# Kernel optimization log

Hardware: AMD Instinct MI355X
Metric: run time of the kernel (lower is better)

## Reference

```python
import jax, jax.numpy as jnp
import numpy as np

KERNEL = 8
WEIGHT_INIT = np.array([0.49403, -0.44625, 0.82544, 0.99267, 1.6915, -2.0835, 2.9114,
                        -5.6555, 3.5984, -10.205, 20.828, -0.0022237, 0.0097854, 157.35],
                       dtype=np.float32)


def setup_inputs() -> dict:
    key = jax.random.key(0)
    x = jax.random.normal(key, (2048, 128, KERNEL, KERNEL), dtype=jnp.float32)
    weight = jnp.asarray(WEIGHT_INIT)
    return {"input": x, "weight": weight}


def reference(input, weight):
    eye = jnp.eye(KERNEL, dtype=input.dtype)  # serves as both mask and eye(8)
    # A = I - x @ x^T  over trailing two dims
    A = eye - jnp.matmul(input, jnp.swapaxes(input, 2, 3))
    B = jnp.matmul(A, A)
    C = jnp.matmul(B, A)
    D = jnp.matmul(C, A)
    E = jnp.matmul(D, A)
    F = jnp.matmul(E, A)
    G = jnp.matmul(F, A)
    Mat = (weight[0] * A + weight[1] * B + weight[2] * C + weight[3] * D
           + weight[4] * E + weight[5] * F + weight[6] * G + weight[7] * eye)
    return input + jnp.matmul(Mat, input)
```

## Files before the change

### kernel.cpp

```cpp
#include <hip/hip_runtime.h>


typedef float v2f __attribute__((ext_vector_type(2)));

__device__ __forceinline__ v2f pk_mul(v2f a, v2f b) {
    v2f d;
    asm("v_pk_mul_f32 %0, %1, %2" : "=v"(d) : "v"(a), "v"(b));
    return d;
}
__device__ __forceinline__ void pk_fma(v2f &acc, v2f a, v2f b) {
    asm("v_pk_fma_f32 %0, %1, %2, %0" : "+v"(acc) : "v"(a), "v"(b));
}
__device__ __forceinline__ v2f pk_mul_lo(v2f a, v2f b) {
    v2f d;
    asm("v_pk_mul_f32 %0, %1, %2 op_sel:[0,0] op_sel_hi:[0,1]"
        : "=v"(d) : "v"(a), "v"(b));
    return d;
}
__device__ __forceinline__ void pk_fma_lo(v2f &acc, v2f a, v2f b) {
    asm("v_pk_fma_f32 %0, %1, %2, %0 op_sel:[0,0,0] op_sel_hi:[0,1,1]"
        : "+v"(acc) : "v"(a), "v"(b));
}
__device__ __forceinline__ void pk_fma_hi(v2f &acc, v2f a, v2f b) {
    asm("v_pk_fma_f32 %0, %1, %2, %0 op_sel:[1,0,0] op_sel_hi:[1,1,1]"
        : "+v"(acc) : "v"(a), "v"(b));
}

__device__ __forceinline__ float pswap(float x)
{
    return __builtin_bit_cast(float,
        __builtin_amdgcn_update_dpp(0, __builtin_bit_cast(int, x),
                                    0xB1, 0xF, 0xF, true));
}

#define SE(p, q) S[(p) < (q) ? (p) : (q)][(p) < (q) ? (q) : (p)]
#define AE(p, q) A[(p) < (q) ? (p) : (q)][(p) < (q) ? (q) : (p)]

#define POW_STEP(wk)                                                      \
    {                                                                     \
        const v2f wv = (v2f){(wk), (wk)};                                 \
        _Pragma("unroll")                                                 \
        for (int j = 0; j < 2; ++j) {                                     \
            v2f n[8];                                                     \
            _Pragma("unroll")                                             \
            for (int p = 0; p < 8; ++p) {                                 \
                v2f a = pk_mul_lo(Ar[p][0], y[j][0]);                     \
                pk_fma_hi(a, Ar[p][0], y[j][1]);                          \
                pk_fma_lo(a, Ar[p][1], y[j][2]);                          \
                pk_fma_hi(a, Ar[p][1], y[j][3]);                          \
                pk_fma_lo(a, Ar[p][2], y[j][4]);                          \
                pk_fma_hi(a, Ar[p][2], y[j][5]);                          \
                pk_fma_lo(a, Ar[p][3], y[j][6]);                          \
                pk_fma_hi(a, Ar[p][3], y[j][7]);                          \
                n[p] = a;                                                 \
            }                                                             \
            _Pragma("unroll")                                             \
            for (int p = 0; p < 8; ++p) {                                 \
                y[j][p] = n[p];                                           \
                pk_fma(acc[j][p], wv, n[p]);                              \
            }                                                             \
        }                                                                 \
    }

__global__ __launch_bounds__(256)
__attribute__((amdgpu_waves_per_eu(2, 8)))
void ns_poly_kernel(const float* __restrict__ in,
                    const float* __restrict__ wp,
                    float* __restrict__ out)
{
    const int tid = threadIdx.x;
    const int m   = blockIdx.x * 128 + (tid >> 1);
    const int h   = tid & 1;

    const float w0 = wp[0], w1 = wp[1], w2 = wp[2], w3 = wp[3];
    const float w4 = wp[4], w5 = wp[5], w6 = wp[6], w7 = wp[7];

    const float* bp      = in + (size_t)m * 64 + h * 4;
    const float* baseOwn = bp + h * 32;
    const float* basePar = bp + (1 - h) * 32;

    v2f y[2][8];
#pragma unroll
    for (int p = 0; p < 4; ++p) {
        const float4 v = *reinterpret_cast<const float4*>(baseOwn + p * 8);
        y[0][p] = (v2f){v.x, v.y};
        y[1][p] = (v2f){v.z, v.w};
    }
#pragma unroll
    for (int p = 0; p < 4; ++p) {
        const float4 v = *reinterpret_cast<const float4*>(basePar + p * 8);
        y[0][4 + p] = (v2f){v.x, v.y};
        y[1][4 + p] = (v2f){v.z, v.w};
    }

    float S[8][8];
#pragma unroll
    for (int p = 0; p < 8; ++p)
#pragma unroll
        for (int q = p; q < 8; ++q) {
            v2f a = pk_mul(y[0][p], y[0][q]);
            pk_fma(a, y[1][p], y[1][q]);
            S[p][q] = a.x + a.y;
        }

    float A[8][8];
#pragma unroll
    for (int p = 0; p < 8; ++p)
#pragma unroll
        for (int q = p; q < 8; ++q) {
            const float other = pswap(SE((p) ^ 4, (q) ^ 4));
            A[p][q] = (p == q ? 1.0f : 0.0f) - S[p][q] - other;
        }

    v2f Ar[8][4];
#pragma unroll
    for (int p = 0; p < 8; ++p)
#pragma unroll
        for (int jq = 0; jq < 4; ++jq)
            Ar[p][jq] = (v2f){AE(p, 2 * jq), AE(p, 2 * jq + 1)};

    v2f acc[2][8];
    const v2f w7v = (v2f){1.0f + w7, 1.0f + w7};
#pragma unroll
    for (int j = 0; j < 2; ++j)
#pragma unroll
        for (int p = 0; p < 8; ++p)
            acc[j][p] = pk_mul(w7v, y[j][p]);

    POW_STEP(w0);
    POW_STEP(w1);
    POW_STEP(w2);
    POW_STEP(w3);
    POW_STEP(w4);
    POW_STEP(w5);
    POW_STEP(w6);

    float* obp     = out + (size_t)m * 64 + h * 4;
    float* oandOwn = obp + h * 32;
    float* oandPar = obp + (1 - h) * 32;
#pragma unroll
    for (int p = 0; p < 4; ++p)
        *reinterpret_cast<float4*>(oandOwn + p * 8) =
            make_float4(acc[0][p].x, acc[0][p].y, acc[1][p].x, acc[1][p].y);
#pragma unroll
    for (int p = 0; p < 4; ++p)
        *reinterpret_cast<float4*>(oandPar + p * 8) =
            make_float4(acc[0][4 + p].x, acc[0][4 + p].y,
                        acc[1][4 + p].x, acc[1][4 + p].y);
}

extern "C" void kernel_launch(void* const* d_in, const int* in_sizes, int n_in,
                              void* d_out, int out_size, void* d_ws, size_t ws_size,
                              hipStream_t stream)
{
    const float* in = (const float*)d_in[0];
    const float* w  = (const float*)d_in[1];
    float* outp     = (float*)d_out;

    const int nmat   = in_sizes[0] / 64;
    const int blocks = nmat / 128;
    ns_poly_kernel<<<blocks, 256, 0, stream>>>(in, w, outp);
}
```

Before: 126.6 us.

## Stage input and output through swizzled LDS for coalesced global access

Each wave now copies its 32 matrices into LDS with fully contiguous float4 global loads, then reads its per-lane row pairs from LDS using an XOR swizzle. The output is staged the same way in reverse. Rows are now read in natural order instead of own/partner order, which simplifies the partner index in the A construction. The goal is to replace strided per-thread global loads and stores with coalesced ones, at the cost of 32KB of LDS per block. The waves_per_eu attribute is also removed, and the LDS handoff depends on lgkmcnt waits within a wave instead of barriers.

After: 119.6 us. -5.5%, faster.

```diff
diff --git a/kernel.cpp b/kernel.cpp
--- a/kernel.cpp
+++ b/kernel.cpp
@@ -33,7 +33,6 @@
                                     0xB1, 0xF, 0xF, true));
 }
 
-#define SE(p, q) S[(p) < (q) ? (p) : (q)][(p) < (q) ? (q) : (p)]
 #define AE(p, q) A[(p) < (q) ? (p) : (q)][(p) < (q) ? (q) : (p)]
 
 #define POW_STEP(wk)                                                      \
@@ -63,34 +62,43 @@
     }
 
 __global__ __launch_bounds__(256)
-__attribute__((amdgpu_waves_per_eu(2, 8)))
 void ns_poly_kernel(const float* __restrict__ in,
                     const float* __restrict__ wp,
                     float* __restrict__ out)
 {
-    const int tid = threadIdx.x;
-    const int m   = blockIdx.x * 128 + (tid >> 1);
-    const int h   = tid & 1;
+    __shared__ float4 lds[2048];
+
+    const int tid  = threadIdx.x;
+    const int wave = tid >> 6;
+    const int lane = tid & 63;
+    const int l    = lane >> 1;
+    const int h    = lane & 1;
 
     const float w0 = wp[0], w1 = wp[1], w2 = wp[2], w3 = wp[3];
     const float w4 = wp[4], w5 = wp[5], w6 = wp[6], w7 = wp[7];
 
-    const float* bp      = in + (size_t)m * 64 + h * 4;
-    const float* baseOwn = bp + h * 32;
-    const float* basePar = bp + (1 - h) * 32;
+    const int wave_mat0 = blockIdx.x * 128 + wave * 32;
+    const float4* __restrict__ gsrc =
+        reinterpret_cast<const float4*>(in) + (size_t)wave_mat0 * 16;
+    float4* __restrict__ gdst =
+        reinterpret_cast<float4*>(out) + (size_t)wave_mat0 * 16;
+    float4* L = lds + wave * 512;
+
+#pragma unroll
+    for (int it = 0; it < 8; ++it) {
+        const int C  = it * 64 + lane;
+        const int Cs = C ^ (((C >> 4) & 3) << 1);
+        L[Cs] = gsrc[C];
+    }
+    asm volatile("s_waitcnt lgkmcnt(0)" ::: "memory");
 
     v2f y[2][8];
 #pragma unroll
-    for (int p = 0; p < 4; ++p) {
-        const float4 v = *reinterpret_cast<const float4*>(baseOwn + p * 8);
-        y[0][p] = (v2f){v.x, v.y};
-        y[1][p] = (v2f){v.z, v.w};
-    }
-#pragma unroll
-    for (int p = 0; p < 4; ++p) {
-        const float4 v = *reinterpret_cast<const float4*>(basePar + p * 8);
-        y[0][4 + p] = (v2f){v.x, v.y};
-        y[1][4 + p] = (v2f){v.z, v.w};
+    for (int g = 0; g < 8; ++g) {
+        const int f4 = (l * 16 + g * 2 + h) ^ ((l & 3) << 1);
+        const float4 v = L[f4];
+        y[0][g] = (v2f){v.x, v.y};
+        y[1][g] = (v2f){v.z, v.w};
     }
 
     float S[8][8];
@@ -108,7 +116,7 @@
     for (int p = 0; p < 8; ++p)
 #pragma unroll
         for (int q = p; q < 8; ++q) {
-            const float other = pswap(SE((p) ^ 4, (q) ^ 4));
+            const float other = pswap(S[p][q]);
             A[p][q] = (p == q ? 1.0f : 0.0f) - S[p][q] - other;
         }
 
@@ -135,18 +143,20 @@
     POW_STEP(w5);
     POW_STEP(w6);
 
-    float* obp     = out + (size_t)m * 64 + h * 4;
-    float* oandOwn = obp + h * 32;
-    float* oandPar = obp + (1 - h) * 32;
 #pragma unroll
-    for (int p = 0; p < 4; ++p)
-        *reinterpret_cast<float4*>(oandOwn + p * 8) =
-            make_float4(acc[0][p].x, acc[0][p].y, acc[1][p].x, acc[1][p].y);
+    for (int g = 0; g < 8; ++g) {
+        const int f4 = (l * 16 + g * 2 + h) ^ ((l & 3) << 1);
+        L[f4] = make_float4(acc[0][g].x, acc[0][g].y,
+                            acc[1][g].x, acc[1][g].y);
+    }
+    asm volatile("s_waitcnt lgkmcnt(0)" ::: "memory");
+
 #pragma unroll
-    for (int p = 0; p < 4; ++p)
-        *reinterpret_cast<float4*>(oandPar + p * 8) =
-            make_float4(acc[0][4 + p].x, acc[0][4 + p].y,
-                        acc[1][4 + p].x, acc[1][4 + p].y);
+    for (int it = 0; it < 8; ++it) {
+        const int C  = it * 64 + lane;
+        const int Cs = C ^ (((C >> 4) & 3) << 1);
+        gdst[C] = L[Cs];
+    }
 }
 
 extern "C" void kernel_launch(void* const* d_in, const int* in_sizes, int n_in,
```
